# Performance work log

Hardware: AMD Instinct MI355X
Metric: run time of the kernel (lower is better)

The kernel has to match this reference:

```python
import jax, jax.numpy as jnp
import numpy as np

BATCH = 8192
HIDDEN = 512
VOCAB = 128
SEQ_LEN = 128  # loop runs SEQ_LEN - 1 steps


def setup_inputs() -> dict:
    key = jax.random.key(0)
    ks = jax.random.split(key, 9)
    s_ih = 1.0 / np.sqrt(HIDDEN)
    inp = {
        "z": jax.random.normal(ks[0], (BATCH, HIDDEN), dtype=jnp.float32),
        # nn.LSTMCell params (gate order: i, f, g, o)
        "W_ih": jax.random.uniform(ks[1], (4 * HIDDEN, VOCAB), jnp.float32, -s_ih, s_ih),
        "W_hh": jax.random.uniform(ks[2], (4 * HIDDEN, HIDDEN), jnp.float32, -s_ih, s_ih),
        "b_ih": jax.random.uniform(ks[3], (4 * HIDDEN,), jnp.float32, -s_ih, s_ih),
        "b_hh": jax.random.uniform(ks[4], (4 * HIDDEN,), jnp.float32, -s_ih, s_ih),
        # cell_state_from_z: Linear(hidden, hidden)
        "W_cz": jax.random.uniform(ks[5], (HIDDEN, HIDDEN), jnp.float32, -s_ih, s_ih),
        "b_cz": jax.random.uniform(ks[6], (HIDDEN,), jnp.float32, -s_ih, s_ih),
        # fc: Linear(hidden, vocab)
        "W_fc": jax.random.uniform(ks[7], (VOCAB, HIDDEN), jnp.float32, -s_ih, s_ih),
        "b_fc": jax.random.uniform(ks[8], (VOCAB,), jnp.float32, -s_ih, s_ih),
    }
    return inp


def reference(z, W_ih, W_hh, b_ih, b_hh, W_cz, b_cz, W_fc, b_fc):
    batch = z.shape[0]
    # learnable cell state from z
    c0 = jax.nn.relu(z @ W_cz.T + b_cz)
    h0 = z
    # start token: one-hot at index 0
    tok0 = jnp.zeros((batch, VOCAB), dtype=z.dtype).at[:, 0].set(1.0)
    b = b_ih + b_hh

    def step(carry, _):
        h, c, tok = carry
        gates = tok @ W_ih.T + h @ W_hh.T + b  # (batch, 4H)
        i, f, g, o = jnp.split(gates, 4, axis=-1)
        i = jax.nn.sigmoid(i)
        f = jax.nn.sigmoid(f)
        g = jnp.tanh(g)
        o = jax.nn.sigmoid(o)
        c_new = f * c + i * g
        h_new = o * jnp.tanh(c_new)
        logits = jax.nn.relu(h_new @ W_fc.T + b_fc)  # (batch, vocab)
        # softmax then argmax == argmax of logits; feed one-hot of greedy token
        tok_new = jax.nn.one_hot(jnp.argmax(logits, axis=-1), VOCAB, dtype=z.dtype)
        return (h_new, c_new, tok_new), logits

    _, out = jax.lax.scan(step, (h0, c0, tok0), None, length=SEQ_LEN - 1)
    return jnp.transpose(out, (1, 0, 2))  # (batch, seq_len-1, vocab)
```

## Files before the change

kernel.cpp:

```cpp
#include <hip/hip_runtime.h>
#include <math.h>
#include <stdint.h>

#define BATCH  8192
#define HIDDEN 512
#define VOCAB  128
#define NSTEP  127
#define OUTROW (NSTEP * VOCAB)
#define NG     2048

using half8   = __attribute__((ext_vector_type(8))) _Float16;
using half4   = __attribute__((ext_vector_type(4))) _Float16;
using float4v = __attribute__((ext_vector_type(4))) float;

#define GLD16(g, l) __builtin_amdgcn_global_load_lds( \
    (const __attribute__((address_space(1))) void*)(g), \
    (__attribute__((address_space(3))) void*)(l), 16, 0, 0)

__device__ __forceinline__ float fast_rcp(float x) { return __builtin_amdgcn_rcpf(x); }
__device__ __forceinline__ float fast_sig(float x) { return fast_rcp(1.0f + __expf(-x)); }
__device__ __forceinline__ float fast_tanh(float x) { return 1.0f - 2.0f * fast_rcp(1.0f + __expf(2.0f * x)); }

__device__ __forceinline__ int orig_row_of(int np) {
    int bn = np >> 7, cc = np & 127;
    int wv = cc >> 6, cw = cc & 63;
    int gate = cw >> 4, jjl = cw & 15;
    int jj = bn * 32 + wv * 16 + jjl;
    return gate * HIDDEN + jj;
}

__global__ __launch_bounds__(256) void init_tok_kernel(int* __restrict__ tok) {
    int i = blockIdx.x * 256 + threadIdx.x;
    if (i < BATCH) tok[i] = 0;
}

__global__ __launch_bounds__(256) void prep_whh_kernel(
    const float* __restrict__ Whh, _Float16* __restrict__ wh, _Float16* __restrict__ wl)
{
    int np = blockIdx.x;
    int orig = orig_row_of(np);
    for (int k = threadIdx.x; k < HIDDEN; k += 256) {
        float w = Whh[(size_t)orig * HIDDEN + k] * 2048.0f;
        _Float16 h = (_Float16)w;
        wh[(size_t)np * HIDDEN + k] = h;
        wl[(size_t)np * HIDDEN + k] = (_Float16)(w - (float)h);
    }
}

__global__ __launch_bounds__(128) void prep_wih_kernel(
    const float* __restrict__ Wih, const float* __restrict__ bih,
    const float* __restrict__ bhh, float* __restrict__ wihT, float* __restrict__ bcomb)
{
    int np = blockIdx.x;
    int orig = orig_row_of(np);
    int v = threadIdx.x;
    wihT[(size_t)v * NG + np] = Wih[(size_t)orig * VOCAB + v];
    if (v == 0) bcomb[np] = bih[orig] + bhh[orig];
}

__global__ __launch_bounds__(256) void prep_wfc_kernel(
    const float* __restrict__ Wfc, _Float16* __restrict__ wh, _Float16* __restrict__ wl)
{
    int i = blockIdx.x * 256 + threadIdx.x;
    float w = Wfc[i] * 2048.0f;
    _Float16 h = (_Float16)w;
    wh[i] = h;
    wl[i] = (_Float16)(w - (float)h);
}

__global__ __launch_bounds__(256) void prep_z_kernel(
    const float* __restrict__ z, _Float16* __restrict__ zh, _Float16* __restrict__ zl)
{
    int i = blockIdx.x * 256 + threadIdx.x;
    float4 v = ((const float4*)z)[i];
    float s0 = v.x * 2048.f, s1 = v.y * 2048.f, s2 = v.z * 2048.f, s3 = v.w * 2048.f;
    _Float16 h0 = (_Float16)s0, h1 = (_Float16)s1, h2 = (_Float16)s2, h3 = (_Float16)s3;
    half4 H = {h0, h1, h2, h3};
    half4 L = {(_Float16)(s0 - (float)h0), (_Float16)(s1 - (float)h1),
               (_Float16)(s2 - (float)h2), (_Float16)(s3 - (float)h3)};
    ((half4*)zh)[i] = H;
    ((half4*)zl)[i] = L;
}

__global__ __launch_bounds__(256) void c0_kernel(
    const float* __restrict__ z, const float* __restrict__ Wcz,
    const float* __restrict__ bcz, float* __restrict__ c)
{
    __shared__ float As[16][128];
    __shared__ float Bs[16][128];
    const int m0 = blockIdx.x * 128;
    const int n0 = blockIdx.y * 128;
    const int tid = threadIdx.x;
    const int ty = tid >> 4, tx = tid & 15;

    float acc[8][8];
#pragma unroll
    for (int i = 0; i < 8; ++i)
#pragma unroll
        for (int j = 0; j < 8; ++j) acc[i][j] = 0.f;

    for (int kc = 0; kc < HIDDEN; kc += 16) {
#pragma unroll
        for (int i = 0; i < 2; ++i) {
            int id = tid * 2 + i;
            int row = id >> 2;
            int kq = (id & 3) * 4;
            float4 av = *(const float4*)(z + (size_t)(m0 + row) * HIDDEN + kc + kq);
            As[kq + 0][row] = av.x; As[kq + 1][row] = av.y;
            As[kq + 2][row] = av.z; As[kq + 3][row] = av.w;
            float4 bv = *(const float4*)(Wcz + (size_t)(n0 + row) * HIDDEN + kc + kq);
            Bs[kq + 0][row] = bv.x; Bs[kq + 1][row] = bv.y;
            Bs[kq + 2][row] = bv.z; Bs[kq + 3][row] = bv.w;
        }
        __syncthreads();
#pragma unroll 4
        for (int k = 0; k < 16; ++k) {
            float a[8], b[8];
            *(float4*)&a[0] = *(const float4*)&As[k][ty * 8];
            *(float4*)&a[4] = *(const float4*)&As[k][ty * 8 + 4];
            *(float4*)&b[0] = *(const float4*)&Bs[k][tx * 8];
            *(float4*)&b[4] = *(const float4*)&Bs[k][tx * 8 + 4];
#pragma unroll
            for (int i = 0; i < 8; ++i)
#pragma unroll
                for (int j = 0; j < 8; ++j)
                    acc[i][j] = fmaf(a[i], b[j], acc[i][j]);
        }
        __syncthreads();
    }
#pragma unroll
    for (int i = 0; i < 8; ++i) {
        int m = m0 + ty * 8 + i;
#pragma unroll
        for (int j = 0; j < 8; ++j) {
            int n = n0 + tx * 8 + j;
            c[(size_t)m * HIDDEN + n] = fmaxf(acc[i][j] + bcz[n], 0.f);
        }
    }
}

__global__ __launch_bounds__(256, 2) void lstm_mfma_kernel(
    const _Float16* __restrict__ hin_h, const _Float16* __restrict__ hin_l,
    const _Float16* __restrict__ whh_h, const _Float16* __restrict__ whh_l,
    const float* __restrict__ wihT, const float* __restrict__ bcomb,
    const int* __restrict__ tok, float* __restrict__ c,
    _Float16* __restrict__ hout_h, _Float16* __restrict__ hout_l)
{
    __shared__ _Float16 As_h[128][32];
    __shared__ _Float16 As_l[128][32];
    __shared__ _Float16 Bs_h[256][32];
    __shared__ _Float16 Bs_l[256][32];

    const int tid  = threadIdx.x;
    const int wid  = tid >> 6, lane = tid & 63;
    const int m0   = blockIdx.x * 128;
    const int n0   = blockIdx.y * 256;

    float4v acc[8][4];
#pragma unroll
    for (int i = 0; i < 8; ++i)
#pragma unroll
        for (int j = 0; j < 4; ++j) acc[i][j] = (float4v){0.f, 0.f, 0.f, 0.f};

    const int lrow = lane >> 2;
    const int lchk = (lane & 3) ^ ((lane >> 3) & 3);
    const int loff = lrow * HIDDEN + lchk * 8;

    const _Float16* agh = hin_h + (size_t)(m0 + wid * 32) * HIDDEN + loff;
    const _Float16* agl = hin_l + (size_t)(m0 + wid * 32) * HIDDEN + loff;
    const _Float16* bgh = whh_h + (size_t)(n0 + wid * 64) * HIDDEN + loff;
    const _Float16* bgl = whh_l + (size_t)(n0 + wid * 64) * HIDDEN + loff;

    const int t = lane & 15, qr = lane >> 4;
    const int qa = (qr ^ ((t >> 1) & 3)) * 8;

    for (int kc = 0; kc < HIDDEN; kc += 32) {
        GLD16(agh + kc,                   &As_h[wid * 32][0]);
        GLD16(agh + kc + 16 * HIDDEN,     &As_h[wid * 32 + 16][0]);
        GLD16(agl + kc,                   &As_l[wid * 32][0]);
        GLD16(agl + kc + 16 * HIDDEN,     &As_l[wid * 32 + 16][0]);
        GLD16(bgh + kc,                   &Bs_h[wid * 64][0]);
        GLD16(bgh + kc + 16 * HIDDEN,     &Bs_h[wid * 64 + 16][0]);
        GLD16(bgh + kc + 32 * HIDDEN,     &Bs_h[wid * 64 + 32][0]);
        GLD16(bgh + kc + 48 * HIDDEN,     &Bs_h[wid * 64 + 48][0]);
        GLD16(bgl + kc,                   &Bs_l[wid * 64][0]);
        GLD16(bgl + kc + 16 * HIDDEN,     &Bs_l[wid * 64 + 16][0]);
        GLD16(bgl + kc + 32 * HIDDEN,     &Bs_l[wid * 64 + 32][0]);
        GLD16(bgl + kc + 48 * HIDDEN,     &Bs_l[wid * 64 + 48][0]);
        __syncthreads();

        half8 bh[4], bl[4];
#pragma unroll
        for (int j = 0; j < 4; ++j) {
            bh[j] = *(const half8*)&Bs_h[wid * 64 + j * 16 + t][qa];
            bl[j] = *(const half8*)&Bs_l[wid * 64 + j * 16 + t][qa];
        }
#pragma unroll
        for (int i = 0; i < 8; ++i) {
            half8 ah = *(const half8*)&As_h[i * 16 + t][qa];
            half8 al = *(const half8*)&As_l[i * 16 + t][qa];
#pragma unroll
            for (int j = 0; j < 4; ++j) {
                acc[i][j] = __builtin_amdgcn_mfma_f32_16x16x32_f16(ah, bh[j], acc[i][j], 0, 0, 0);
                acc[i][j] = __builtin_amdgcn_mfma_f32_16x16x32_f16(ah, bl[j], acc[i][j], 0, 0, 0);
                acc[i][j] = __builtin_amdgcn_mfma_f32_16x16x32_f16(al, bh[j], acc[i][j], 0, 0, 0);
            }
        }
        __syncthreads();
    }

    const float INV22 = 1.0f / 4194304.0f;
    const int g  = blockIdx.y * 4 + wid;
    const int jj = (g >> 1) * 32 + (g & 1) * 16 + t;
    const int colb = n0 + wid * 64 + t;
    float bias[4];
    int   col[4];
#pragma unroll
    for (int j = 0; j < 4; ++j) {
        col[j]  = colb + j * 16;
        bias[j] = bcomb[col[j]];
    }
#pragma unroll
    for (int i = 0; i < 8; ++i) {
        int mb = m0 + i * 16 + qr * 4;
#pragma unroll
        for (int r = 0; r < 4; ++r) {
            int m  = mb + r;
            int tk = tok[m];
            const float* wv = wihT + (size_t)tk * NG;
            float iv = acc[i][0][r] * INV22 + bias[0] + wv[col[0]];
            float fv = acc[i][1][r] * INV22 + bias[1] + wv[col[1]];
            float gv = acc[i][2][r] * INV22 + bias[2] + wv[col[2]];
            float ov = acc[i][3][r] * INV22 + bias[3] + wv[col[3]];
            float ig = fast_sig(iv);
            float fg = fast_sig(fv);
            float gg = fast_tanh(gv);
            float og = fast_sig(ov);
            size_t ci = (size_t)m * HIDDEN + jj;
            float cn = fg * c[ci] + ig * gg;
            c[ci] = cn;
            float hn = og * fast_tanh(cn);
            float hs = hn * 2048.f;
            _Float16 hh = (_Float16)hs;
            hout_h[ci] = hh;
            hout_l[ci] = (_Float16)(hs - (float)hh);
        }
    }
}

__global__ __launch_bounds__(128) void logits_mfma_kernel(
    const _Float16* __restrict__ hh_, const _Float16* __restrict__ hl_,
    const _Float16* __restrict__ wfc_h, const _Float16* __restrict__ wfc_l,
    const float* __restrict__ b_fc, float* __restrict__ out_t, int* __restrict__ tok)
{
    __shared__ _Float16 Ah[32][64];
    __shared__ _Float16 Al[32][64];
    __shared__ _Float16 Bh[128][64];
    __shared__ _Float16 Bl[128][64];

    const int tid = threadIdx.x;
    const int wid = tid >> 6, lane = tid & 63;
    const int m0  = blockIdx.x * 32;
    const int t   = lane & 15, qr = lane >> 4;

    float4v acc[8];
#pragma unroll
    for (int j = 0; j < 8; ++j) acc[j] = (float4v){0.f, 0.f, 0.f, 0.f};

    const int lrow = lane >> 3;
    const int lchk = (lane & 7) ^ lrow;
    const int loff = lrow * HIDDEN + lchk * 8;

    const _Float16* Ag = (wid == 0 ? hh_ : hl_) + (size_t)m0 * HIDDEN + loff;
    _Float16* Adst = (wid == 0) ? &Ah[0][0] : &Al[0][0];
    const _Float16* Bgh = wfc_h + (size_t)(wid * 64) * HIDDEN + loff;
    const _Float16* Bgl = wfc_l + (size_t)(wid * 64) * HIDDEN + loff;

    const int sa = t & 7;

    for (int kc = 0; kc < HIDDEN; kc += 64) {
#pragma unroll
        for (int s = 0; s < 4; ++s)
            GLD16(Ag + kc + s * 8 * HIDDEN, Adst + (s * 8) * 64);
#pragma unroll
        for (int s = 0; s < 8; ++s) {
            GLD16(Bgh + kc + s * 8 * HIDDEN, &Bh[wid * 64 + s * 8][0]);
            GLD16(Bgl + kc + s * 8 * HIDDEN, &Bl[wid * 64 + s * 8][0]);
        }
        __syncthreads();
#pragma unroll
        for (int kh = 0; kh < 2; ++kh) {
            int q = kh * 4 + qr;
            int arow = wid * 16 + t;
            half8 a_h = *(const half8*)&Ah[arow][(q ^ sa) * 8];
            half8 a_l = *(const half8*)&Al[arow][(q ^ sa) * 8];
#pragma unroll
            for (int j = 0; j < 8; ++j) {
                half8 b_h = *(const half8*)&Bh[j * 16 + t][(q ^ sa) * 8];
                half8 b_l = *(const half8*)&Bl[j * 16 + t][(q ^ sa) * 8];
                acc[j] = __builtin_amdgcn_mfma_f32_16x16x32_f16(a_h, b_h, acc[j], 0, 0, 0);
                acc[j] = __builtin_amdgcn_mfma_f32_16x16x32_f16(a_h, b_l, acc[j], 0, 0, 0);
                acc[j] = __builtin_amdgcn_mfma_f32_16x16x32_f16(a_l, b_h, acc[j], 0, 0, 0);
            }
        }
        __syncthreads();
    }

    const float INV22 = 1.0f / 4194304.0f;
    float bv[8];
#pragma unroll
    for (int j = 0; j < 8; ++j) bv[j] = b_fc[j * 16 + t];

#pragma unroll
    for (int r = 0; r < 4; ++r) {
        int m = m0 + wid * 16 + qr * 4 + r;
        float vals[8];
        float vbest = -1.0f; int ibest = 0;
#pragma unroll
        for (int j = 0; j < 8; ++j) {
            float x = fmaxf(acc[j][r] * INV22 + bv[j], 0.f);
            vals[j] = x;
            if (x > vbest) { vbest = x; ibest = j * 16 + t; }
        }
        float* op = out_t + (size_t)m * OUTROW;
#pragma unroll
        for (int j = 0; j < 8; ++j) op[j * 16 + t] = vals[j];
#pragma unroll
        for (int d = 1; d < 16; d <<= 1) {
            float vo = __shfl_xor(vbest, d, 64);
            int   io = __shfl_xor(ibest, d, 64);
            if (vo > vbest || (vo == vbest && io < ibest)) { vbest = vo; ibest = io; }
        }
        if (t == 0) tok[m] = ibest;
    }
}

extern "C" void kernel_launch(void* const* d_in, const int* in_sizes, int n_in,
                              void* d_out, int out_size, void* d_ws, size_t ws_size,
                              hipStream_t stream)
{
    const float* z    = (const float*)d_in[0];
    const float* W_ih = (const float*)d_in[1];
    const float* W_hh = (const float*)d_in[2];
    const float* b_ih = (const float*)d_in[3];
    const float* b_hh = (const float*)d_in[4];
    const float* W_cz = (const float*)d_in[5];
    const float* b_cz = (const float*)d_in[6];
    const float* W_fc = (const float*)d_in[7];
    const float* b_fc = (const float*)d_in[8];
    float* out = (float*)d_out;

    uint8_t* p = (uint8_t*)d_ws;
    float* c = (float*)p;            p += (size_t)BATCH * HIDDEN * 4;
    _Float16* sA_h = (_Float16*)p;   p += (size_t)BATCH * HIDDEN * 2;
    _Float16* sA_l = (_Float16*)p;   p += (size_t)BATCH * HIDDEN * 2;
    _Float16* sB_h = (_Float16*)p;   p += (size_t)BATCH * HIDDEN * 2;
    _Float16* sB_l = (_Float16*)p;   p += (size_t)BATCH * HIDDEN * 2;
    _Float16* whhh = (_Float16*)p;   p += (size_t)NG * HIDDEN * 2;
    _Float16* whhl = (_Float16*)p;   p += (size_t)NG * HIDDEN * 2;
    _Float16* wfch = (_Float16*)p;   p += (size_t)VOCAB * HIDDEN * 2;
    _Float16* wfcl = (_Float16*)p;   p += (size_t)VOCAB * HIDDEN * 2;
    float* wihT  = (float*)p;        p += (size_t)VOCAB * NG * 4;
    float* bcomb = (float*)p;        p += (size_t)NG * 4;
    int* tokp    = (int*)p;          p += (size_t)BATCH * 4;

    init_tok_kernel<<<BATCH / 256, 256, 0, stream>>>(tokp);
    prep_whh_kernel<<<NG, 256, 0, stream>>>(W_hh, whhh, whhl);
    prep_wih_kernel<<<NG, 128, 0, stream>>>(W_ih, b_ih, b_hh, wihT, bcomb);
    prep_wfc_kernel<<<(VOCAB * HIDDEN) / 256, 256, 0, stream>>>(W_fc, wfch, wfcl);
    prep_z_kernel<<<(BATCH * HIDDEN / 4) / 256, 256, 0, stream>>>(z, sA_h, sA_l);
    c0_kernel<<<dim3(BATCH / 128, HIDDEN / 128), 256, 0, stream>>>(z, W_cz, b_cz, c);

    for (int t = 0; t < NSTEP; ++t) {
        const _Float16* inh = (t & 1) ? sB_h : sA_h;
        const _Float16* inl = (t & 1) ? sB_l : sA_l;
        _Float16* outh = (t & 1) ? sA_h : sB_h;
        _Float16* outl = (t & 1) ? sA_l : sB_l;
        lstm_mfma_kernel<<<dim3(BATCH / 128, NG / 256), 256, 0, stream>>>(
            inh, inl, whhh, whhl, wihT, bcomb, tokp, c, outh, outl);
        logits_mfma_kernel<<<BATCH / 32, 128, 0, stream>>>(
            outh, outl, wfch, wfcl, b_fc, out + (size_t)t * VOCAB, tokp);
    }
}
```

Baseline: 8.489 ms.

## Load weight operands directly to registers and repack W_ih gates as float4

Both the LSTM and logits kernels now read the W_hh / W_fc fp16 B-operands straight from global memory into registers instead of staging them through LDS. This cuts shared memory use and LDS traffic, but relies on the L2 cache to serve the repeated weight reads. W_ih and the combined bias are repacked so the four gates of a hidden unit sit in one float4, giving a single gather per row. Token indices are cached in shared memory. The logits kernel is re-tiled so each wave covers 64 vocab columns for 32 rows, with a cross-wave argmax reduction through shared memory.

```diff
diff --git a/kernel.cpp b/kernel.cpp
--- a/kernel.cpp
+++ b/kernel.cpp
@@ -47,15 +47,26 @@
     }
 }
 
-__global__ __launch_bounds__(128) void prep_wih_kernel(
+__global__ __launch_bounds__(128) void prep_wih4_kernel(
     const float* __restrict__ Wih, const float* __restrict__ bih,
-    const float* __restrict__ bhh, float* __restrict__ wihT, float* __restrict__ bcomb)
-{
-    int np = blockIdx.x;
-    int orig = orig_row_of(np);
-    int v = threadIdx.x;
-    wihT[(size_t)v * NG + np] = Wih[(size_t)orig * VOCAB + v];
-    if (v == 0) bcomb[np] = bih[orig] + bhh[orig];
+    const float* __restrict__ bhh, float4* __restrict__ wih4, float4* __restrict__ bcomb4)
+{
+    int jj = blockIdx.x;
+    int v  = threadIdx.x;
+    float4 w;
+    w.x = Wih[(size_t)(0 * HIDDEN + jj) * VOCAB + v];
+    w.y = Wih[(size_t)(1 * HIDDEN + jj) * VOCAB + v];
+    w.z = Wih[(size_t)(2 * HIDDEN + jj) * VOCAB + v];
+    w.w = Wih[(size_t)(3 * HIDDEN + jj) * VOCAB + v];
+    wih4[(size_t)v * HIDDEN + jj] = w;
+    if (v == 0) {
+        float4 b;
+        b.x = bih[0 * HIDDEN + jj] + bhh[0 * HIDDEN + jj];
+        b.y = bih[1 * HIDDEN + jj] + bhh[1 * HIDDEN + jj];
+        b.z = bih[2 * HIDDEN + jj] + bhh[2 * HIDDEN + jj];
+        b.w = bih[3 * HIDDEN + jj] + bhh[3 * HIDDEN + jj];
+        bcomb4[jj] = b;
+    }
 }
 
 __global__ __launch_bounds__(256) void prep_wfc_kernel(
@@ -142,14 +153,13 @@
 __global__ __launch_bounds__(256, 2) void lstm_mfma_kernel(
     const _Float16* __restrict__ hin_h, const _Float16* __restrict__ hin_l,
     const _Float16* __restrict__ whh_h, const _Float16* __restrict__ whh_l,
-    const float* __restrict__ wihT, const float* __restrict__ bcomb,
+    const float4* __restrict__ wih4, const float4* __restrict__ bcomb4,
     const int* __restrict__ tok, float* __restrict__ c,
     _Float16* __restrict__ hout_h, _Float16* __restrict__ hout_l)
 {
     __shared__ _Float16 As_h[128][32];
     __shared__ _Float16 As_l[128][32];
-    __shared__ _Float16 Bs_h[256][32];
-    __shared__ _Float16 Bs_l[256][32];
+    __shared__ int tok_s[128];
 
     const int tid  = threadIdx.x;
     const int wid  = tid >> 6, lane = tid & 63;
@@ -162,39 +172,34 @@
 #pragma unroll
         for (int j = 0; j < 4; ++j) acc[i][j] = (float4v){0.f, 0.f, 0.f, 0.f};
 
+    if (tid < 128) tok_s[tid] = tok[m0 + tid];
+
     const int lrow = lane >> 2;
     const int lchk = (lane & 3) ^ ((lane >> 3) & 3);
     const int loff = lrow * HIDDEN + lchk * 8;
-
     const _Float16* agh = hin_h + (size_t)(m0 + wid * 32) * HIDDEN + loff;
     const _Float16* agl = hin_l + (size_t)(m0 + wid * 32) * HIDDEN + loff;
-    const _Float16* bgh = whh_h + (size_t)(n0 + wid * 64) * HIDDEN + loff;
-    const _Float16* bgl = whh_l + (size_t)(n0 + wid * 64) * HIDDEN + loff;
 
     const int t = lane & 15, qr = lane >> 4;
     const int qa = (qr ^ ((t >> 1) & 3)) * 8;
 
+    const _Float16* bgh = whh_h + (size_t)(n0 + wid * 64 + t) * HIDDEN + qr * 8;
+    const _Float16* bgl = whh_l + (size_t)(n0 + wid * 64 + t) * HIDDEN + qr * 8;
+
     for (int kc = 0; kc < HIDDEN; kc += 32) {
-        GLD16(agh + kc,                   &As_h[wid * 32][0]);
-        GLD16(agh + kc + 16 * HIDDEN,     &As_h[wid * 32 + 16][0]);
-        GLD16(agl + kc,                   &As_l[wid * 32][0]);
-        GLD16(agl + kc + 16 * HIDDEN,     &As_l[wid * 32 + 16][0]);
-        GLD16(bgh + kc,                   &Bs_h[wid * 64][0]);
-        GLD16(bgh + kc + 16 * HIDDEN,     &Bs_h[wid * 64 + 16][0]);
-        GLD16(bgh + kc + 32 * HIDDEN,     &Bs_h[wid * 64 + 32][0]);
-        GLD16(bgh + kc + 48 * HIDDEN,     &Bs_h[wid * 64 + 48][0]);
-        GLD16(bgl + kc,                   &Bs_l[wid * 64][0]);
-        GLD16(bgl + kc + 16 * HIDDEN,     &Bs_l[wid * 64 + 16][0]);
-        GLD16(bgl + kc + 32 * HIDDEN,     &Bs_l[wid * 64 + 32][0]);
-        GLD16(bgl + kc + 48 * HIDDEN,     &Bs_l[wid * 64 + 48][0]);
-        __syncthreads();
+        GLD16(agh + kc,               &As_h[wid * 32][0]);
+        GLD16(agh + kc + 16 * HIDDEN, &As_h[wid * 32 + 16][0]);
+        GLD16(agl + kc,               &As_l[wid * 32][0]);
+        GLD16(agl + kc + 16 * HIDDEN, &As_l[wid * 32 + 16][0]);
 
         half8 bh[4], bl[4];
 #pragma unroll
         for (int j = 0; j < 4; ++j) {
-            bh[j] = *(const half8*)&Bs_h[wid * 64 + j * 16 + t][qa];
-            bl[j] = *(const half8*)&Bs_l[wid * 64 + j * 16 + t][qa];
-        }
+            bh[j] = *(const half8*)(bgh + (size_t)j * 16 * HIDDEN + kc);
+            bl[j] = *(const half8*)(bgl + (size_t)j * 16 * HIDDEN + kc);
+        }
+        __syncthreads();
+
 #pragma unroll
         for (int i = 0; i < 8; ++i) {
             half8 ah = *(const half8*)&As_h[i * 16 + t][qa];
@@ -212,26 +217,22 @@
     const float INV22 = 1.0f / 4194304.0f;
     const int g  = blockIdx.y * 4 + wid;
     const int jj = (g >> 1) * 32 + (g & 1) * 16 + t;
-    const int colb = n0 + wid * 64 + t;
-    float bias[4];
-    int   col[4];
-#pragma unroll
-    for (int j = 0; j < 4; ++j) {
-        col[j]  = colb + j * 16;
-        bias[j] = bcomb[col[j]];
-    }
+    const float4 b4 = bcomb4[jj];
+    const float4* wjj = wih4 + jj;
+
 #pragma unroll
     for (int i = 0; i < 8; ++i) {
-        int mb = m0 + i * 16 + qr * 4;
+        int mb = i * 16 + qr * 4;
 #pragma unroll
         for (int r = 0; r < 4; ++r) {
-            int m  = mb + r;
-            int tk = tok[m];
-            const float* wv = wihT + (size_t)tk * NG;
-            float iv = acc[i][0][r] * INV22 + bias[0] + wv[col[0]];
-            float fv = acc[i][1][r] * INV22 + bias[1] + wv[col[1]];
-            float gv = acc[i][2][r] * INV22 + bias[2] + wv[col[2]];
-            float ov = acc[i][3][r] * INV22 + bias[3] + wv[col[3]];
+            int ml = mb + r;
+            int m  = m0 + ml;
+            int tk = tok_s[ml];
+            float4 w4 = wjj[(size_t)tk * HIDDEN];
+            float iv = acc[i][0][r] * INV22 + b4.x + w4.x;
+            float fv = acc[i][1][r] * INV22 + b4.y + w4.y;
+            float gv = acc[i][2][r] * INV22 + b4.z + w4.z;
+            float ov = acc[i][3][r] * INV22 + b4.w + w4.w;
             float ig = fast_sig(iv);
             float fg = fast_sig(fv);
             float gg = fast_tanh(gv);
@@ -255,83 +256,98 @@
 {
     __shared__ _Float16 Ah[32][64];
     __shared__ _Float16 Al[32][64];
-    __shared__ _Float16 Bh[128][64];
-    __shared__ _Float16 Bl[128][64];
+    __shared__ float redv[32][2];
+    __shared__ int   redi[32][2];
 
     const int tid = threadIdx.x;
     const int wid = tid >> 6, lane = tid & 63;
     const int m0  = blockIdx.x * 32;
     const int t   = lane & 15, qr = lane >> 4;
 
-    float4v acc[8];
-#pragma unroll
-    for (int j = 0; j < 8; ++j) acc[j] = (float4v){0.f, 0.f, 0.f, 0.f};
+    float4v acc[2][4];
+#pragma unroll
+    for (int im = 0; im < 2; ++im)
+#pragma unroll
+        for (int j = 0; j < 4; ++j) acc[im][j] = (float4v){0.f, 0.f, 0.f, 0.f};
 
     const int lrow = lane >> 3;
     const int lchk = (lane & 7) ^ lrow;
     const int loff = lrow * HIDDEN + lchk * 8;
-
     const _Float16* Ag = (wid == 0 ? hh_ : hl_) + (size_t)m0 * HIDDEN + loff;
     _Float16* Adst = (wid == 0) ? &Ah[0][0] : &Al[0][0];
-    const _Float16* Bgh = wfc_h + (size_t)(wid * 64) * HIDDEN + loff;
-    const _Float16* Bgl = wfc_l + (size_t)(wid * 64) * HIDDEN + loff;
 
     const int sa = t & 7;
+
+    const _Float16* bgh = wfc_h + (size_t)(wid * 64 + t) * HIDDEN + qr * 8;
+    const _Float16* bgl = wfc_l + (size_t)(wid * 64 + t) * HIDDEN + qr * 8;
 
     for (int kc = 0; kc < HIDDEN; kc += 64) {
 #pragma unroll
         for (int s = 0; s < 4; ++s)
             GLD16(Ag + kc + s * 8 * HIDDEN, Adst + (s * 8) * 64);
-#pragma unroll
-        for (int s = 0; s < 8; ++s) {
-            GLD16(Bgh + kc + s * 8 * HIDDEN, &Bh[wid * 64 + s * 8][0]);
-            GLD16(Bgl + kc + s * 8 * HIDDEN, &Bl[wid * 64 + s * 8][0]);
-        }
-        __syncthreads();
+
+        half8 bh[4][2], bl[4][2];
+#pragma unroll
+        for (int j = 0; j < 4; ++j)
+#pragma unroll
+            for (int kh = 0; kh < 2; ++kh) {
+                bh[j][kh] = *(const half8*)(bgh + (size_t)j * 16 * HIDDEN + kc + kh * 32);
+                bl[j][kh] = *(const half8*)(bgl + (size_t)j * 16 * HIDDEN + kc + kh * 32);
+            }
+        __syncthreads();
+
 #pragma unroll
         for (int kh = 0; kh < 2; ++kh) {
             int q = kh * 4 + qr;
-            int arow = wid * 16 + t;
-            half8 a_h = *(const half8*)&Ah[arow][(q ^ sa) * 8];
-            half8 a_l = *(const half8*)&Al[arow][(q ^ sa) * 8];
-#pragma unroll
-            for (int j = 0; j < 8; ++j) {
-                half8 b_h = *(const half8*)&Bh[j * 16 + t][(q ^ sa) * 8];
-                half8 b_l = *(const half8*)&Bl[j * 16 + t][(q ^ sa) * 8];
-                acc[j] = __builtin_amdgcn_mfma_f32_16x16x32_f16(a_h, b_h, acc[j], 0, 0, 0);
-                acc[j] = __builtin_amdgcn_mfma_f32_16x16x32_f16(a_h, b_l, acc[j], 0, 0, 0);
-                acc[j] = __builtin_amdgcn_mfma_f32_16x16x32_f16(a_l, b_h, acc[j], 0, 0, 0);
+#pragma unroll
+            for (int im = 0; im < 2; ++im) {
+                half8 a_h = *(const half8*)&Ah[im * 16 + t][(q ^ sa) * 8];
+                half8 a_l = *(const half8*)&Al[im * 16 + t][(q ^ sa) * 8];
+#pragma unroll
+                for (int j = 0; j < 4; ++j) {
+                    acc[im][j] = __builtin_amdgcn_mfma_f32_16x16x32_f16(a_h, bh[j][kh], acc[im][j], 0, 0, 0);
+                    acc[im][j] = __builtin_amdgcn_mfma_f32_16x16x32_f16(a_h, bl[j][kh], acc[im][j], 0, 0, 0);
+                    acc[im][j] = __builtin_amdgcn_mfma_f32_16x16x32_f16(a_l, bh[j][kh], acc[im][j], 0, 0, 0);
+                }
             }
         }
         __syncthreads();
     }
 
     const float INV22 = 1.0f / 4194304.0f;
-    float bv[8];
-#pragma unroll
-    for (int j = 0; j < 8; ++j) bv[j] = b_fc[j * 16 + t];
-
-#pragma unroll
-    for (int r = 0; r < 4; ++r) {
-        int m = m0 + wid * 16 + qr * 4 + r;
-        float vals[8];
-        float vbest = -1.0f; int ibest = 0;
-#pragma unroll
-        for (int j = 0; j < 8; ++j) {
-            float x = fmaxf(acc[j][r] * INV22 + bv[j], 0.f);
-            vals[j] = x;
-            if (x > vbest) { vbest = x; ibest = j * 16 + t; }
-        }
-        float* op = out_t + (size_t)m * OUTROW;
-#pragma unroll
-        for (int j = 0; j < 8; ++j) op[j * 16 + t] = vals[j];
-#pragma unroll
-        for (int d = 1; d < 16; d <<= 1) {
-            float vo = __shfl_xor(vbest, d, 64);
-            int   io = __shfl_xor(ibest, d, 64);
-            if (vo > vbest || (vo == vbest && io < ibest)) { vbest = vo; ibest = io; }
-        }
-        if (t == 0) tok[m] = ibest;
+    float bv[4];
+#pragma unroll
+    for (int j = 0; j < 4; ++j) bv[j] = b_fc[wid * 64 + j * 16 + t];
+
+#pragma unroll
+    for (int im = 0; im < 2; ++im) {
+#pragma unroll
+        for (int r = 0; r < 4; ++r) {
+            int row = im * 16 + qr * 4 + r;
+            int m   = m0 + row;
+            float vbest = -1.0f; int ibest = 0;
+            float* op = out_t + (size_t)m * OUTROW + wid * 64 + t;
+#pragma unroll
+            for (int j = 0; j < 4; ++j) {
+                float x = fmaxf(acc[im][j][r] * INV22 + bv[j], 0.f);
+                op[j * 16] = x;
+                int col = wid * 64 + j * 16 + t;
+                if (x > vbest) { vbest = x; ibest = col; }
+            }
+#pragma unroll
+            for (int d = 1; d < 16; d <<= 1) {
+                float vo = __shfl_xor(vbest, d, 64);
+                int   io = __shfl_xor(ibest, d, 64);
+                if (vo > vbest || (vo == vbest && io < ibest)) { vbest = vo; ibest = io; }
+            }
+            if (t == 0) { redv[row][wid] = vbest; redi[row][wid] = ibest; }
+        }
+    }
+    __syncthreads();
+    if (tid < 32) {
+        float v0 = redv[tid][0], v1 = redv[tid][1];
+        int   i0 = redi[tid][0], i1 = redi[tid][1];
+        tok[m0 + tid] = (v1 > v0) ? i1 : i0;
     }
 }
 
@@ -360,13 +376,13 @@
     _Float16* whhl = (_Float16*)p;   p += (size_t)NG * HIDDEN * 2;
     _Float16* wfch = (_Float16*)p;   p += (size_t)VOCAB * HIDDEN * 2;
     _Float16* wfcl = (_Float16*)p;   p += (size_t)VOCAB * HIDDEN * 2;
-    float* wihT  = (float*)p;        p += (size_t)VOCAB * NG * 4;
-    float* bcomb = (float*)p;        p += (size_t)NG * 4;
-    int* tokp    = (int*)p;          p += (size_t)BATCH * 4;
+    float4* wih4   = (float4*)p;     p += (size_t)VOCAB * HIDDEN * 16;
+    float4* bcomb4 = (float4*)p;     p += (size_t)HIDDEN * 16;
+    int* tokp      = (int*)p;        p += (size_t)BATCH * 4;
 
     init_tok_kernel<<<BATCH / 256, 256, 0, stream>>>(tokp);
     prep_whh_kernel<<<NG, 256, 0, stream>>>(W_hh, whhh, whhl);
-    prep_wih_kernel<<<NG, 128, 0, stream>>>(W_ih, b_ih, b_hh, wihT, bcomb);
+    prep_wih4_kernel<<<HIDDEN, 128, 0, stream>>>(W_ih, b_ih, b_hh, wih4, bcomb4);
     prep_wfc_kernel<<<(VOCAB * HIDDEN) / 256, 256, 0, stream>>>(W_fc, wfch, wfcl);
     prep_z_kernel<<<(BATCH * HIDDEN / 4) / 256, 256, 0, stream>>>(z, sA_h, sA_l);
     c0_kernel<<<dim3(BATCH / 128, HIDDEN / 128), 256, 0, stream>>>(z, W_cz, b_cz, c);
@@ -377,7 +393,7 @@
         _Float16* outh = (t & 1) ? sA_h : sB_h;
         _Float16* outl = (t & 1) ? sA_l : sB_l;
         lstm_mfma_kernel<<<dim3(BATCH / 128, NG / 256), 256, 0, stream>>>(
-            inh, inl, whhh, whhl, wihT, bcomb, tokp, c, outh, outl);
+            inh, inl, whhh, whhl, wih4, bcomb4, tokp, c, outh, outl);
         logits_mfma_kernel<<<BATCH / 32, 128, 0, stream>>>(
             outh, outl, wfch, wfcl, b_fc, out + (size_t)t * VOCAB, tokp);
     }
```

Result: slower. 8.988 ms (+5.9%).
